# Kernel tuning notes

Measured on AMD Instinct MI355X. Metric: run time of the kernel, lower is better.

Reference implementation:

```python
import jax, jax.numpy as jnp
import numpy as np
import math

B, S, D = 1, 4096, 512
H, KVH, DH = 8, 4, 64
DH2 = DH // 2
M = int(math.isqrt(S))           # product-key grid side, S == M*M
K = 8                            # top_k
ROPE_BASE = 10000.0


def rope_cos_sin(seq_len, dh, base):
    inv_freq = 1.0 / (base ** (jnp.arange(0, dh, 2, dtype=jnp.float32) / dh))
    t = jnp.arange(seq_len, dtype=jnp.float32)
    freqs = jnp.outer(t, inv_freq)                      # (S, dh/2)
    emb = jnp.concatenate([freqs, freqs], axis=-1)      # (S, dh)
    return jnp.cos(emb), jnp.sin(emb)


def apply_rope(x, cos, sin):
    # x: (B, H, S, dh); half-split rotation (llama-style)
    dh2 = x.shape[-1] // 2
    rot = jnp.concatenate([-x[..., dh2:], x[..., :dh2]], axis=-1)
    return x * cos + rot * sin


def setup_inputs() -> dict:
    key = jax.random.key(0)
    ks = jax.random.split(key, 5)
    s = 0.02
    x = jax.random.normal(ks[0], (B, S, D), dtype=jnp.float32)
    Wq = jax.random.normal(ks[1], (H * DH, D), dtype=jnp.float32) * s
    Wk = jax.random.normal(ks[2], (KVH * DH, D), dtype=jnp.float32) * s
    Wv = jax.random.normal(ks[3], (KVH * DH, D), dtype=jnp.float32) * s
    Wo = jax.random.normal(ks[4], (D, H * DH), dtype=jnp.float32) * s
    return {"x": x, "Wq": Wq, "Wk": Wk, "Wv": Wv, "Wo": Wo}


def reference(x, Wq, Wk, Wv, Wo):
    b, s, d = x.shape
    cos, sin = rope_cos_sin(s, DH, ROPE_BASE)
    q = (x @ Wq.T).reshape(b, s, H, DH).transpose(0, 2, 1, 3)      # (B,H,S,DH)
    k = (x @ Wk.T).reshape(b, s, KVH, DH).transpose(0, 2, 1, 3)    # (B,KVH,S,DH)
    v = (x @ Wv.T).reshape(b, s, KVH, DH).transpose(0, 2, 1, 3)
    q = apply_rope(q, cos, sin)
    k = apply_rope(k, cos, sin)
    rep = H // KVH                                                 # GQA repeat_kv
    k = jnp.repeat(k, rep, axis=1)                                 # (B,H,S,DH)
    v = jnp.repeat(v, rep, axis=1)

    # factorized product keys: sum over grid rows / cols
    kg = k.reshape(b, H, M, M, DH)
    k1 = kg[..., :DH2].sum(axis=-2)                                # (B,H,M,DH2)
    k2 = kg[..., DH2:].sum(axis=-3)                                # (B,H,M,DH2)
    q1, q2 = q[..., :DH2], q[..., DH2:]

    def topk_sel(qh, kh):  # qh: (S,DH2), kh: (M,DH2)
        scores = qh @ kh.T                                         # (S,M)
        _, idx = jax.lax.top_k(scores, K)                          # (S,K)
        return kh[idx], idx                                        # (S,K,DH2), (S,K)

    sel2 = jax.vmap(jax.vmap(topk_sel))
    k1v, i1 = sel2(q1, k1)                                         # (B,H,S,K,DH2)
    k2v, i2 = sel2(q2, k2)

    # cross-product candidates: (B,H,S,K,K,DH) -> (B,H,S,K*K,DH)
    c1 = jnp.broadcast_to(k1v[:, :, :, :, None, :], (b, H, s, K, K, DH2))
    c2 = jnp.broadcast_to(k2v[:, :, :, None, :, :], (b, H, s, K, K, DH2))
    cand = jnp.concatenate([c1, c2], axis=-1).reshape(b, H, s, K * K, DH)

    scores_final = jnp.einsum('bhsd,bhscd->bhsc', q, cand)         # (B,H,S,K*K)
    _, sel = jax.lax.top_k(scores_final, K)                        # (B,H,S,K)
    final_k = jnp.take_along_axis(cand, sel[..., None], axis=3)    # (B,H,S,K,DH)

    row = jnp.take_along_axis(i1, sel // K, axis=3)
    col = jnp.take_along_axis(i2, sel % K, axis=3)
    v_idx = row * M + col                                          # (B,H,S,K)
    final_v = jax.vmap(jax.vmap(lambda vb, ib: vb[ib]))(v, v_idx)  # (B,H,S,K,DH)

    attn = jax.nn.softmax(
        jnp.einsum('bhsd,bhskd->bhsk', q, final_k) / math.sqrt(DH), axis=-1)
    o = jnp.einsum('bhsk,bhskd->bhsd', attn, final_v)              # (B,H,S,DH)
    o = o.transpose(0, 2, 1, 3).reshape(b, s, H * DH)
    return o @ Wo.T
```

## Files before the change

kernel.cpp:

```cpp
#include <hip/hip_runtime.h>
#include <math.h>


static constexpr size_t OFF_P1   = 0;
static constexpr size_t OFF_P2   = 4194304;
static constexpr size_t OFF_KB   = 8388608;
static constexpr size_t OFF_V    = 9437184;
static constexpr size_t OFF_COS  = 10485760;
static constexpr size_t OFF_SIN  = 10616832;
static constexpr size_t OFF_K1   = 10747904;
static constexpr size_t OFF_K2   = 10756096;
static constexpr size_t OFF_O    = 10764288;
static constexpr size_t OFF_PACK = 12861440;

#define LDB 132
#define TILE_F (16 * LDB)

__device__ __forceinline__ float rdlane_f(float v, int lane) {
  return __int_as_float(__builtin_amdgcn_readlane(__float_as_int(v), lane));
}

__global__ __launch_bounds__(512) void pre_kernel(const float* __restrict__ A,
    const float* __restrict__ Wq, const float* __restrict__ Wk,
    const float* __restrict__ Wv, float* __restrict__ C1,
    float* __restrict__ C2, float* __restrict__ cosT,
    float* __restrict__ sinT) {
  __shared__ float As[2 * TILE_F];
  __shared__ float Bs[2 * TILE_F];
  const int bid = blockIdx.x;
  const int tid = threadIdx.x;
  if (bid >= 512) {
    int idx = (bid - 512) * 512 + tid;
    int s = idx >> 5;
    int dp = idx & 31;
    double e = (double)dp * (1.0 / 32.0);
    float pf = (float)pow(10000.0, e);
    float invf = 1.0f / pf;
    float argf = __fmul_rn((float)s, invf);
    cosT[idx] = (float)cos((double)argf);
    sinT[idx] = (float)sin((double)argf);
    return;
  }
  const int bn = bid & 7;
  const int bm = (bid >> 3) & 31;
  const int z = bid >> 8;
  const int k0 = z ? 384 : 0;
  const int k1 = z ? 512 : 384;
  float* __restrict__ C = z ? C2 : C1;
  const int lrow = tid >> 2;
  const int lko = (tid & 3) << 2;
  const int ty = tid >> 4;
  const int tx = tid & 15;
  const float* Bbase = (bn < 4) ? (Wq + ((size_t)bn * 128) * 512)
                     : (bn < 6) ? (Wk + ((size_t)(bn - 4) * 128) * 512)
                                : (Wv + ((size_t)(bn - 6) * 128) * 512);
  const float* Ap = A + (size_t)(bm * 128 + lrow) * 512 + lko;
  const float* Bp = Bbase + (size_t)lrow * 512 + lko;
  float acc[4][8] = {{0.f}};
  float4 a0 = *(const float4*)(Ap + k0);
  float4 b0 = *(const float4*)(Bp + k0);
  int p = 0;
  for (int kt = k0; kt < k1; kt += 16) {
    float* Asp = As + p * TILE_F;
    float* Bsp = Bs + p * TILE_F;
    Asp[(lko + 0) * LDB + lrow] = a0.x;
    Asp[(lko + 1) * LDB + lrow] = a0.y;
    Asp[(lko + 2) * LDB + lrow] = a0.z;
    Asp[(lko + 3) * LDB + lrow] = a0.w;
    Bsp[(lko + 0) * LDB + lrow] = b0.x;
    Bsp[(lko + 1) * LDB + lrow] = b0.y;
    Bsp[(lko + 2) * LDB + lrow] = b0.z;
    Bsp[(lko + 3) * LDB + lrow] = b0.w;
    __syncthreads();
    if (kt + 16 < k1) {
      a0 = *(const float4*)(Ap + kt + 16);
      b0 = *(const float4*)(Bp + kt + 16);
    }
    #pragma unroll
    for (int k = 0; k < 16; ++k) {
      float4 av = *(const float4*)(&Asp[k * LDB + (ty << 2)]);
      float4 bl = *(const float4*)(&Bsp[k * LDB + (tx << 2)]);
      float4 bh = *(const float4*)(&Bsp[k * LDB + 64 + (tx << 2)]);
      float af[4] = {av.x, av.y, av.z, av.w};
      float bf[8] = {bl.x, bl.y, bl.z, bl.w, bh.x, bh.y, bh.z, bh.w};
      #pragma unroll
      for (int i2 = 0; i2 < 4; ++i2)
        #pragma unroll
        for (int j2 = 0; j2 < 8; ++j2)
          acc[i2][j2] = fmaf(af[i2], bf[j2], acc[i2][j2]);
    }
    p ^= 1;
  }
  #pragma unroll
  for (int i2 = 0; i2 < 4; ++i2) {
    int row = bm * 128 + (ty << 2) + i2;
    float* Cp = C + (size_t)row * 1024 + bn * 128;
    *(float4*)(Cp + (tx << 2))      = make_float4(acc[i2][0], acc[i2][1], acc[i2][2], acc[i2][3]);
    *(float4*)(Cp + 64 + (tx << 2)) = make_float4(acc[i2][4], acc[i2][5], acc[i2][6], acc[i2][7]);
  }
}

__global__ __launch_bounds__(256) void gemm128_out(const float* __restrict__ A,
    const float* __restrict__ B, float* __restrict__ Cbase, int N) {
  __shared__ float As[2 * TILE_F];
  __shared__ float Bs[2 * TILE_F];
  const int tid = threadIdx.x;
  const int z = blockIdx.z;
  const int k0 = z << 7;
  const int k1 = k0 + 128;
  float* __restrict__ C = Cbase + (size_t)z * ((size_t)4096 * N);
  const int bm = blockIdx.y, bn = blockIdx.x;
  const int lrow = tid >> 1;
  const int lko = (tid & 1) << 3;
  const int ty = tid >> 4;
  const int tx = tid & 15;
  const float* Ap = A + (size_t)(bm * 128 + lrow) * 512 + lko;
  const float* Bp = B + (size_t)(bn * 128 + lrow) * 512 + lko;
  float acc[8][8] = {{0.f}};
  float4 a0 = *(const float4*)(Ap + k0);
  float4 a1 = *(const float4*)(Ap + k0 + 4);
  float4 b0 = *(const float4*)(Bp + k0);
  float4 b1 = *(const float4*)(Bp + k0 + 4);
  int p = 0;
  for (int kt = k0; kt < k1; kt += 16) {
    float* Asp = As + p * TILE_F;
    float* Bsp = Bs + p * TILE_F;
    Asp[(lko + 0) * LDB + lrow] = a0.x;
    Asp[(lko + 1) * LDB + lrow] = a0.y;
    Asp[(lko + 2) * LDB + lrow] = a0.z;
    Asp[(lko + 3) * LDB + lrow] = a0.w;
    Asp[(lko + 4) * LDB + lrow] = a1.x;
    Asp[(lko + 5) * LDB + lrow] = a1.y;
    Asp[(lko + 6) * LDB + lrow] = a1.z;
    Asp[(lko + 7) * LDB + lrow] = a1.w;
    Bsp[(lko + 0) * LDB + lrow] = b0.x;
    Bsp[(lko + 1) * LDB + lrow] = b0.y;
    Bsp[(lko + 2) * LDB + lrow] = b0.z;
    Bsp[(lko + 3) * LDB + lrow] = b0.w;
    Bsp[(lko + 4) * LDB + lrow] = b1.x;
    Bsp[(lko + 5) * LDB + lrow] = b1.y;
    Bsp[(lko + 6) * LDB + lrow] = b1.z;
    Bsp[(lko + 7) * LDB + lrow] = b1.w;
    __syncthreads();
    if (kt + 16 < k1) {
      a0 = *(const float4*)(Ap + kt + 16);
      a1 = *(const float4*)(Ap + kt + 20);
      b0 = *(const float4*)(Bp + kt + 16);
      b1 = *(const float4*)(Bp + kt + 20);
    }
    #pragma unroll
    for (int k = 0; k < 16; ++k) {
      float4 al = *(const float4*)(&Asp[k * LDB + (ty << 2)]);
      float4 ah = *(const float4*)(&Asp[k * LDB + 64 + (ty << 2)]);
      float4 bl = *(const float4*)(&Bsp[k * LDB + (tx << 2)]);
      float4 bh = *(const float4*)(&Bsp[k * LDB + 64 + (tx << 2)]);
      float af[8] = {al.x, al.y, al.z, al.w, ah.x, ah.y, ah.z, ah.w};
      float bf[8] = {bl.x, bl.y, bl.z, bl.w, bh.x, bh.y, bh.z, bh.w};
      #pragma unroll
      for (int i2 = 0; i2 < 8; ++i2)
        #pragma unroll
        for (int j2 = 0; j2 < 8; ++j2)
          acc[i2][j2] = fmaf(af[i2], bf[j2], acc[i2][j2]);
    }
    p ^= 1;
  }
  #pragma unroll
  for (int i2 = 0; i2 < 8; ++i2) {
    int row = bm * 128 + ((i2 < 4) ? (ty << 2) + i2 : 64 + (ty << 2) + i2 - 4);
    float* Cp = C + (size_t)row * N + bn * 128;
    *(float4*)(Cp + (tx << 2))      = make_float4(acc[i2][0], acc[i2][1], acc[i2][2], acc[i2][3]);
    *(float4*)(Cp + 64 + (tx << 2)) = make_float4(acc[i2][4], acc[i2][5], acc[i2][6], acc[i2][7]);
  }
}

__global__ __launch_bounds__(256) void combine4_kernel(const float* __restrict__ o0,
    const float* __restrict__ o1, const float* __restrict__ o2,
    const float* __restrict__ o3, float* __restrict__ out) {
  int i = blockIdx.x * 256 + threadIdx.x;
  out[i] = __fadd_rn(__fadd_rn(__fadd_rn(o0[i], o1[i]), o2[i]), o3[i]);
}

__global__ __launch_bounds__(256) void kv_rope_kernel(const float* __restrict__ p1,
    const float* __restrict__ p2, const float* __restrict__ cosT,
    const float* __restrict__ sinT, float* __restrict__ kb,
    float* __restrict__ vb) {
  int id = blockIdx.x * 256 + threadIdx.x;
  int s = id >> 9;
  int n = 512 + (id & 511);
  int idx = (s << 10) + n;
  float val = __fadd_rn(p1[idx], p2[idx]);
  int d = n & 63;
  if (n < 768) {
    int pidx = idx ^ 32;
    float pv = __fadd_rn(p1[pidx], p2[pidx]);
    float cs = cosT[(s << 5) + (d & 31)];
    float sn = sinT[(s << 5) + (d & 31)];
    float rot = (d < 32) ? -pv : pv;
    float out = __fadd_rn(__fmul_rn(val, cs), __fmul_rn(rot, sn));
    int kvh = (n - 512) >> 6;
    kb[((size_t)(kvh * 4096 + s) << 6) + d] = out;
  } else {
    int kvh = (n - 768) >> 6;
    vb[((size_t)(kvh * 4096 + s) << 6) + d] = val;
  }
}

__global__ __launch_bounds__(256) void k12_np_kernel(const float* __restrict__ kb,
    float* __restrict__ k1t, float* __restrict__ k2t) {
  int id = blockIdx.x * 256 + threadIdx.x;
  int which = id >> 13;
  int rem = id & 8191;
  int kvh = rem >> 11;
  int rem2 = rem & 2047;
  int i = rem2 >> 5;
  int d = rem2 & 31;
  const float* base = kb + ((size_t)(kvh * 4096) << 6);
  if (which == 0) {
    float acc = base[((size_t)(i * 64) << 6) + d];
    for (int c = 1; c < 64; ++c)
      acc = __fadd_rn(acc, base[((size_t)(i * 64 + c) << 6) + d]);
    k1t[(kvh * 64 + i) * 32 + d] = acc;
  } else {
    float acc = base[((size_t)i << 6) + d + 32];
    for (int r = 1; r < 64; ++r)
      acc = __fadd_rn(acc, base[((size_t)(r * 64 + i) << 6) + d + 32]);
    k2t[(kvh * 64 + i) * 32 + d] = acc;
  }
}

__global__ __launch_bounds__(256) void stage1_sel_kernel(
    const float* __restrict__ p1, const float* __restrict__ p2,
    const float* __restrict__ cosT, const float* __restrict__ sinT,
    const float* __restrict__ k1t, const float* __restrict__ k2t,
    unsigned long long* __restrict__ packs) {
  __shared__ float smem[8704];
  float* qs = smem;
  float* kd = smem + 4352;
  const int t = threadIdx.x;
  const int h = blockIdx.y;
  const int s0 = blockIdx.x * 64;
  const int kvh = h >> 1;
  #pragma unroll
  for (int i = 0; i < 16; ++i) {
    int j = t + i * 256;
    int ss = j >> 6, d = j & 63;
    int s = s0 + ss;
    int idx = (s << 10) + (h << 6) + d;
    float val = __fadd_rn(p1[idx], p2[idx]);
    float pv  = __fadd_rn(p1[idx ^ 32], p2[idx ^ 32]);
    float cs = cosT[(s << 5) + (d & 31)];
    float sn = sinT[(s << 5) + (d & 31)];
    float rot = (d < 32) ? -pv : pv;
    qs[d * 68 + ss] = __fadd_rn(__fmul_rn(val, cs), __fmul_rn(rot, sn));
  }
  #pragma unroll
  for (int i = 0; i < 8; ++i) {
    int j = t + i * 256;
    int r = j >> 5, d = j & 31;
    kd[d * 132 + r]      = k1t[(kvh * 64 + r) * 32 + d];
    kd[d * 132 + 64 + r] = k2t[(kvh * 64 + r) * 32 + d];
  }
  __syncthreads();
  const int ty = t >> 4;
  const int tx = t & 15;
  float acc1[4][4] = {{0.f}};
  float acc2[4][4] = {{0.f}};
  #pragma unroll
  for (int dp = 0; dp < 32; ++dp) {
    float4 kv1 = *(const float4*)&kd[dp * 132 + (ty << 2)];
    float4 kv2 = *(const float4*)&kd[dp * 132 + 64 + (ty << 2)];
    float4 q1 = *(const float4*)&qs[dp * 68 + (tx << 2)];
    float4 q2 = *(const float4*)&qs[(32 + dp) * 68 + (tx << 2)];
    float k1f[4] = {kv1.x, kv1.y, kv1.z, kv1.w};
    float k2f[4] = {kv2.x, kv2.y, kv2.z, kv2.w};
    float q1f[4] = {q1.x, q1.y, q1.z, q1.w};
    float q2f[4] = {q2.x, q2.y, q2.z, q2.w};
    #pragma unroll
    for (int i2 = 0; i2 < 4; ++i2)
      #pragma unroll
      for (int j2 = 0; j2 < 4; ++j2) {
        acc1[i2][j2] = fmaf(k1f[i2], q1f[j2], acc1[i2][j2]);
        acc2[i2][j2] = fmaf(k2f[i2], q2f[j2], acc2[i2][j2]);
      }
  }
  __syncthreads();
  float* sct = smem;
  #pragma unroll
  for (int i2 = 0; i2 < 4; ++i2) {
    int r = (ty << 2) + i2;
    *(float4*)&sct[(size_t)r * 68 + (tx << 2)] =
        make_float4(acc1[i2][0], acc1[i2][1], acc1[i2][2], acc1[i2][3]);
    *(float4*)&sct[(size_t)(64 + r) * 68 + (tx << 2)] =
        make_float4(acc2[i2][0], acc2[i2][1], acc2[i2][2], acc2[i2][3]);
  }
  __syncthreads();
  if (t < 128) {
    int set = t >> 6;
    int sq = t & 63;
    const float* p = sct + (size_t)(set << 6) * 68 + sq;
    float top[8];
    int idx[8];
    #pragma unroll
    for (int u = 0; u < 8; ++u) { top[u] = -INFINITY; idx[u] = 0; }
    #pragma unroll
    for (int r = 0; r < 64; ++r) {
      float v = p[(size_t)r * 68];
      int i = r;
      #pragma unroll
      for (int j = 0; j < 8; ++j) {
        bool gt = v > top[j];
        float tv = top[j]; int ti = idx[j];
        top[j] = gt ? v : tv;
        idx[j] = gt ? i : ti;
        v = gt ? tv : v;
        i = gt ? ti : i;
      }
    }
    unsigned long long pp = 0;
    #pragma unroll
    for (int u = 0; u < 8; ++u) pp |= (unsigned long long)idx[u] << (6 * u);
    packs[(((size_t)(h * 4096 + s0 + sq)) << 1) + set] = pp;
  }
}

__device__ __forceinline__ void bitonic64_val_desc(float& v, int lane) {
  #pragma unroll
  for (int k = 2; k <= 64; k <<= 1) {
    #pragma unroll
    for (int j = k >> 1; j >= 1; j >>= 1) {
      float ov = __shfl_xor(v, j, 64);
      bool up = ((lane & k) == 0) == ((lane & j) == 0);
      float mx = fmaxf(v, ov), mn = fminf(v, ov);
      v = up ? mx : mn;
    }
  }
}

__global__ __launch_bounds__(256) void attn_sel2_kernel(
    const ulonglong2* __restrict__ packs, const float* __restrict__ p1,
    const float* __restrict__ p2, const float* __restrict__ cosT,
    const float* __restrict__ sinT, const float* __restrict__ vb,
    const float* __restrict__ k1t, const float* __restrict__ k2t,
    float* __restrict__ ob) {
  const int lane = threadIdx.x & 63;
  const int w = blockIdx.x * 4 + (threadIdx.x >> 6);
  const int h = w >> 12;
  const int s = w & 4095;
  const int kvh = h >> 1;
  ulonglong2 pk = packs[w];
  const unsigned long long pack1 = pk.x, pack2 = pk.y;
  int qidx = (s << 10) + (h << 6) + lane;
  float vraw = __fadd_rn(p1[qidx], p2[qidx]);
  float pv = __shfl_xor(vraw, 32, 64);
  float cs = cosT[(s << 5) + (lane & 31)];
  float sn = sinT[(s << 5) + (lane & 31)];
  float rot = (lane < 32) ? -pv : pv;
  const float qv = __fadd_rn(__fmul_rn(vraw, cs), __fmul_rn(rot, sn));

  int r1 = (int)((pack1 >> (6 * (lane >> 3))) & 63);
  int r2 = (int)((pack2 >> (6 * (lane & 7))) & 63);
  const float* k1p = k1t + (size_t)(kvh * 64 + r1) * 32;
  const float* k2p = k2t + (size_t)(kvh * 64 + r2) * 32;
  float c = 0.f;
  #pragma unroll
  for (int dq = 0; dq < 32; dq += 4) {
    float4 kk = *(const float4*)(k1p + dq);
    c = __fadd_rn(c, __fmul_rn(rdlane_f(qv, dq + 0), kk.x));
    c = __fadd_rn(c, __fmul_rn(rdlane_f(qv, dq + 1), kk.y));
    c = __fadd_rn(c, __fmul_rn(rdlane_f(qv, dq + 2), kk.z));
    c = __fadd_rn(c, __fmul_rn(rdlane_f(qv, dq + 3), kk.w));
  }
  #pragma unroll
  for (int dq = 0; dq < 32; dq += 4) {
    float4 kk = *(const float4*)(k2p + dq);
    c = __fadd_rn(c, __fmul_rn(rdlane_f(qv, 32 + dq + 0), kk.x));
    c = __fadd_rn(c, __fmul_rn(rdlane_f(qv, 32 + dq + 1), kk.y));
    c = __fadd_rn(c, __fmul_rn(rdlane_f(qv, 32 + dq + 2), kk.z));
    c = __fadd_rn(c, __fmul_rn(rdlane_f(qv, 32 + dq + 3), kk.w));
  }
  const float scand = c;
  float v3 = c;
  bitonic64_val_desc(v3, lane);
  float cvs[8]; int ccs[8];
  unsigned long long used = 0;
  #pragma unroll
  for (int t = 0; t < 8; ++t) {
    float tv = rdlane_f(v3, t);
    unsigned long long m = __ballot(scand == tv) & ~used;
    int ix = __ffsll((long long)m) - 1;
    used |= 1ull << ix;
    cvs[t] = tv;
    ccs[t] = ix;
  }
  float y[8];
  #pragma unroll
  for (int t = 0; t < 8; ++t) y[t] = cvs[t] * 0.125f;
  float mx = y[0];
  #pragma unroll
  for (int t = 1; t < 8; ++t) if (y[t] > mx) mx = y[t];
  float e[8];
  #pragma unroll
  for (int t = 0; t < 8; ++t) e[t] = __expf(__fsub_rn(y[t], mx));
  float wsum = __fadd_rn(__fadd_rn(__fadd_rn(e[0], e[1]), __fadd_rn(e[2], e[3])),
                         __fadd_rn(__fadd_rn(e[4], e[5]), __fadd_rn(e[6], e[7])));
  const float* vbh = vb + ((size_t)kvh << 18);
  float o = 0.f;
  #pragma unroll
  for (int t = 0; t < 8; ++t) {
    float att = __fdiv_rn(e[t], wsum);
    int row = (int)((pack1 >> (6 * (ccs[t] >> 3))) & 63);
    int col = (int)((pack2 >> (6 * (ccs[t] & 7))) & 63);
    o = __fadd_rn(o, __fmul_rn(att, vbh[((size_t)(row * 64 + col) << 6) + lane]));
  }
  ob[(size_t)s * 512 + (h << 6) + lane] = o;
}

extern "C" void kernel_launch(void* const* d_in, const int* in_sizes, int n_in,
                              void* d_out, int out_size, void* d_ws, size_t ws_size,
                              hipStream_t stream) {
  const float* x  = (const float*)d_in[0];
  const float* Wq = (const float*)d_in[1];
  const float* Wk = (const float*)d_in[2];
  const float* Wv = (const float*)d_in[3];
  const float* Wo = (const float*)d_in[4];
  float* ws = (float*)d_ws;
  float* p1   = ws + OFF_P1;
  float* p2   = ws + OFF_P2;
  float* kb   = ws + OFF_KB;
  float* vb   = ws + OFF_V;
  float* cosT = ws + OFF_COS;
  float* sinT = ws + OFF_SIN;
  float* k1t  = ws + OFF_K1;
  float* k2t  = ws + OFF_K2;
  float* ob   = ws + OFF_O;
  unsigned long long* packs = (unsigned long long*)(ws + OFF_PACK);
  float* op = ws + OFF_P1;

  pre_kernel<<<768, 512, 0, stream>>>(x, Wq, Wk, Wv, p1, p2, cosT, sinT);
  kv_rope_kernel<<<8192, 256, 0, stream>>>(p1, p2, cosT, sinT, kb, vb);
  k12_np_kernel<<<64, 256, 0, stream>>>(kb, k1t, k2t);
  stage1_sel_kernel<<<dim3(64, 8), 256, 0, stream>>>(p1, p2, cosT, sinT, k1t, k2t, packs);
  attn_sel2_kernel<<<8192, 256, 0, stream>>>((const ulonglong2*)packs, p1, p2,
                                             cosT, sinT, vb, k1t, k2t, ob);
  gemm128_out<<<dim3(4, 32, 4), 256, 0, stream>>>(ob, Wo, op, 512);
  combine4_kernel<<<8192, 256, 0, stream>>>(op, op + 2097152, op + 4194304,
                                            op + 6291456, (float*)d_out);
}
```

Measured before the change: 236.0 us.

## Vectorize small elementwise kernels and fold V reduction into stage1 launch

The combine and K-RoPE kernels now move float4 per thread instead of one float, which cuts the thread count by four. The V split-K reduction leaves the RoPE kernel and runs in extra blocks appended to the stage1 selection launch, so it overlaps with selection work. The k12 kernel now uses 64-thread blocks across 256 blocks, which spreads its serial column sums over more CUs. Together these reduce launch overhead and make the memory-bound helper kernels cheaper, at the cost of more complex block dispatch in stage1.

```diff
diff --git a/kernel.cpp b/kernel.cpp
--- a/kernel.cpp
+++ b/kernel.cpp
@@ -177,37 +177,53 @@
     const float* __restrict__ o1, const float* __restrict__ o2,
     const float* __restrict__ o3, float* __restrict__ out) {
   int i = blockIdx.x * 256 + threadIdx.x;
-  out[i] = __fadd_rn(__fadd_rn(__fadd_rn(o0[i], o1[i]), o2[i]), o3[i]);
-}
-
-__global__ __launch_bounds__(256) void kv_rope_kernel(const float* __restrict__ p1,
+  float4 a = ((const float4*)o0)[i];
+  float4 b = ((const float4*)o1)[i];
+  float4 c = ((const float4*)o2)[i];
+  float4 d = ((const float4*)o3)[i];
+  float4 r;
+  r.x = __fadd_rn(__fadd_rn(__fadd_rn(a.x, b.x), c.x), d.x);
+  r.y = __fadd_rn(__fadd_rn(__fadd_rn(a.y, b.y), c.y), d.y);
+  r.z = __fadd_rn(__fadd_rn(__fadd_rn(a.z, b.z), c.z), d.z);
+  r.w = __fadd_rn(__fadd_rn(__fadd_rn(a.w, b.w), c.w), d.w);
+  ((float4*)out)[i] = r;
+}
+
+__global__ __launch_bounds__(256) void kv_rope_k(const float* __restrict__ p1,
     const float* __restrict__ p2, const float* __restrict__ cosT,
-    const float* __restrict__ sinT, float* __restrict__ kb,
-    float* __restrict__ vb) {
+    const float* __restrict__ sinT, float* __restrict__ kb) {
   int id = blockIdx.x * 256 + threadIdx.x;
-  int s = id >> 9;
-  int n = 512 + (id & 511);
+  int s = id >> 6;
+  int g = id & 63;
+  int n = 512 + (g << 2);
   int idx = (s << 10) + n;
-  float val = __fadd_rn(p1[idx], p2[idx]);
-  int d = n & 63;
-  if (n < 768) {
-    int pidx = idx ^ 32;
-    float pv = __fadd_rn(p1[pidx], p2[pidx]);
-    float cs = cosT[(s << 5) + (d & 31)];
-    float sn = sinT[(s << 5) + (d & 31)];
-    float rot = (d < 32) ? -pv : pv;
-    float out = __fadd_rn(__fmul_rn(val, cs), __fmul_rn(rot, sn));
-    int kvh = (n - 512) >> 6;
-    kb[((size_t)(kvh * 4096 + s) << 6) + d] = out;
-  } else {
-    int kvh = (n - 768) >> 6;
-    vb[((size_t)(kvh * 4096 + s) << 6) + d] = val;
-  }
-}
-
-__global__ __launch_bounds__(256) void k12_np_kernel(const float* __restrict__ kb,
+  const float4 v1 = *(const float4*)(p1 + idx);
+  const float4 v2 = *(const float4*)(p2 + idx);
+  const float4 q1 = *(const float4*)(p1 + (idx ^ 32));
+  const float4 q2 = *(const float4*)(p2 + (idx ^ 32));
+  int d0 = n & 63;
+  const float4 cs = *(const float4*)(cosT + (s << 5) + (d0 & 31));
+  const float4 sn = *(const float4*)(sinT + (s << 5) + (d0 & 31));
+  float sgn = (d0 < 32) ? -1.0f : 1.0f;
+  float4 out;
+  {
+    float val = __fadd_rn(v1.x, v2.x), pv = __fadd_rn(q1.x, q2.x);
+    out.x = __fadd_rn(__fmul_rn(val, cs.x), __fmul_rn((d0 < 32) ? -pv : pv, sn.x));
+    val = __fadd_rn(v1.y, v2.y); pv = __fadd_rn(q1.y, q2.y);
+    out.y = __fadd_rn(__fmul_rn(val, cs.y), __fmul_rn((d0 < 32) ? -pv : pv, sn.y));
+    val = __fadd_rn(v1.z, v2.z); pv = __fadd_rn(q1.z, q2.z);
+    out.z = __fadd_rn(__fmul_rn(val, cs.z), __fmul_rn((d0 < 32) ? -pv : pv, sn.z));
+    val = __fadd_rn(v1.w, v2.w); pv = __fadd_rn(q1.w, q2.w);
+    out.w = __fadd_rn(__fmul_rn(val, cs.w), __fmul_rn((d0 < 32) ? -pv : pv, sn.w));
+  }
+  (void)sgn;
+  int kvh = (n - 512) >> 6;
+  *(float4*)(kb + (((size_t)(kvh * 4096 + s)) << 6) + d0) = out;
+}
+
+__global__ __launch_bounds__(64) void k12_np_kernel(const float* __restrict__ kb,
     float* __restrict__ k1t, float* __restrict__ k2t) {
-  int id = blockIdx.x * 256 + threadIdx.x;
+  int id = blockIdx.x * 64 + threadIdx.x;
   int which = id >> 13;
   int rem = id & 8191;
   int kvh = rem >> 11;
@@ -232,13 +248,32 @@
     const float* __restrict__ p1, const float* __restrict__ p2,
     const float* __restrict__ cosT, const float* __restrict__ sinT,
     const float* __restrict__ k1t, const float* __restrict__ k2t,
-    unsigned long long* __restrict__ packs) {
+    unsigned long long* __restrict__ packs, float* __restrict__ vb) {
   __shared__ float smem[8704];
+  const int bid = blockIdx.x;
+  const int t = threadIdx.x;
+  if (bid >= 512) {
+    int vid = (bid - 512) * 256 + t;
+    int s = vid >> 6;
+    int g = vid & 63;
+    int n = 768 + (g << 2);
+    int idx = (s << 10) + n;
+    const float4 v1 = *(const float4*)(p1 + idx);
+    const float4 v2 = *(const float4*)(p2 + idx);
+    float4 r;
+    r.x = __fadd_rn(v1.x, v2.x);
+    r.y = __fadd_rn(v1.y, v2.y);
+    r.z = __fadd_rn(v1.z, v2.z);
+    r.w = __fadd_rn(v1.w, v2.w);
+    int kvh = (n - 768) >> 6;
+    int d0 = n & 63;
+    *(float4*)(vb + (((size_t)(kvh * 4096 + s)) << 6) + d0) = r;
+    return;
+  }
   float* qs = smem;
   float* kd = smem + 4352;
-  const int t = threadIdx.x;
-  const int h = blockIdx.y;
-  const int s0 = blockIdx.x * 64;
+  const int h = bid >> 6;
+  const int s0 = (bid & 63) * 64;
   const int kvh = h >> 1;
   #pragma unroll
   for (int i = 0; i < 16; ++i) {
@@ -437,12 +472,13 @@
   float* op = ws + OFF_P1;
 
   pre_kernel<<<768, 512, 0, stream>>>(x, Wq, Wk, Wv, p1, p2, cosT, sinT);
-  kv_rope_kernel<<<8192, 256, 0, stream>>>(p1, p2, cosT, sinT, kb, vb);
-  k12_np_kernel<<<64, 256, 0, stream>>>(kb, k1t, k2t);
-  stage1_sel_kernel<<<dim3(64, 8), 256, 0, stream>>>(p1, p2, cosT, sinT, k1t, k2t, packs);
+  kv_rope_k<<<1024, 256, 0, stream>>>(p1, p2, cosT, sinT, kb);
+  k12_np_kernel<<<256, 64, 0, stream>>>(kb, k1t, k2t);
+  stage1_sel_kernel<<<1536, 256, 0, stream>>>(p1, p2, cosT, sinT, k1t, k2t,
+                                              packs, vb);
   attn_sel2_kernel<<<8192, 256, 0, stream>>>((const ulonglong2*)packs, p1, p2,
                                              cosT, sinT, vb, k1t, k2t, ob);
   gemm128_out<<<dim3(4, 32, 4), 256, 0, stream>>>(ob, Wo, op, 512);
-  combine4_kernel<<<8192, 256, 0, stream>>>(op, op + 2097152, op + 4194304,
+  combine4_kernel<<<2048, 256, 0, stream>>>(op, op + 2097152, op + 4194304,
                                             op + 6291456, (float*)d_out);
 }
```

New measurement: 224.9 us. 1.05x faster.
